# Optimization experiments

Hardware: AMD Instinct MI355X
Metric: run time of the kernel (lower is better)

The kernel has to match this reference:

```python
import jax, jax.numpy as jnp
import numpy as np

EPS = 1e-5

def _ln(x):
    # non-affine LayerNorm over last dim
    m = jnp.mean(x, axis=-1, keepdims=True)
    v = jnp.var(x, axis=-1, keepdims=True)
    return (x - m) / jnp.sqrt(v + EPS)

def setup_inputs() -> dict:
    key = jax.random.key(0)
    ks = jax.random.split(key, 6)
    B, D_in, H = 16384, 512, 512
    bound_i = 1.0 / np.sqrt(D_in)
    bound_h = 1.0 / np.sqrt(H)
    x = jax.random.normal(ks[0], (B, D_in), dtype=jnp.float32)
    hx = jax.random.normal(ks[1], (B, H), dtype=jnp.float32)
    W_i2h = jax.random.uniform(ks[2], (3 * H, D_in), minval=-bound_i, maxval=bound_i, dtype=jnp.float32)
    b_i2h = jax.random.uniform(ks[3], (3 * H,), minval=-bound_i, maxval=bound_i, dtype=jnp.float32)
    W_h2h = jax.random.uniform(ks[4], (3 * H, H), minval=-bound_h, maxval=bound_h, dtype=jnp.float32)
    b_h2h = jax.random.uniform(ks[5], (3 * H,), minval=-bound_h, maxval=bound_h, dtype=jnp.float32)
    return {"x": x, "hx": hx, "W_i2h": W_i2h, "b_i2h": b_i2h, "W_h2h": W_h2h, "b_h2h": b_h2h}

def reference(x, hx, W_i2h, b_i2h, W_h2h, b_h2h):
    H = hx.shape[-1]
    xt = x @ W_i2h.T + b_i2h        # [B, 3H]
    ht = hx @ W_h2h.T + b_h2h       # [B, 3H]
    x_new = xt[:, 2 * H:]
    h_new = ht[:, 2 * H:]
    gates = jax.nn.sigmoid(_ln(xt[:, : 2 * H]) + _ln(ht[:, : 2 * H]))
    r_t = gates[:, :H]
    z_t = gates[:, H:]
    n_t = jnp.tanh(_ln(x_new) + r_t * _ln(h_new))
    h_t = z_t * hx + (1.0 - z_t) * n_t
    return h_t
```

## Files before the change

### kernel.cpp

```cpp
#include <hip/hip_runtime.h>

#define M_ROWS 16384
#define N_COLS 1536
#define K_DIM  512
#define H_DIM  512

typedef __attribute__((ext_vector_type(8))) short short8;
typedef __attribute__((ext_vector_type(16))) float f32x16;

__device__ __forceinline__ unsigned short f2bf(float f) {
  unsigned u = __float_as_uint(f);
  u += 0x7fffu + ((u >> 16) & 1u);
  return (unsigned short)(u >> 16);
}
__device__ __forceinline__ float bf2f(unsigned short h) {
  return __uint_as_float(((unsigned)h) << 16);
}
__device__ __forceinline__ unsigned cvt_pk_bf16(float lo, float hi) {
  unsigned r;
  asm("v_cvt_pk_bf16_f32 %0, %1, %2" : "=v"(r) : "v"(lo), "v"(hi));
  return r;
}

__device__ __forceinline__ void gload_lds16(const void* g, void* l) {
  __builtin_amdgcn_global_load_lds((const __attribute__((address_space(1))) void*)g,
                                   (__attribute__((address_space(3))) void*)l,
                                   16, 0, 0);
}

__global__ __launch_bounds__(256) void cvt_w(
    const float* __restrict__ Wi, const float* __restrict__ Wh,
    unsigned short* __restrict__ Wib, unsigned short* __restrict__ Whb) {
  int i = blockIdx.x * blockDim.x + threadIdx.x;
  const float* s; unsigned short* d; int off;
  if (i < 196608) { s = Wi; d = Wib; off = i; }
  else            { s = Wh; d = Whb; off = i - 196608; }
  float4 f = ((const float4*)s)[off];
  ushort4 u;
  u.x = f2bf(f.x); u.y = f2bf(f.y); u.z = f2bf(f.z); u.w = f2bf(f.w);
  ((ushort4*)d)[off] = u;
}

__global__ __launch_bounds__(512, 1) void fused(
    const float* __restrict__ x, const float* __restrict__ hx,
    const unsigned short* __restrict__ Wib, const unsigned short* __restrict__ Whb,
    const float* __restrict__ b_i2h, const float* __restrict__ b_h2h,
    unsigned short* __restrict__ xt, unsigned short* __restrict__ ht,
    float* __restrict__ out) {
  const int m0 = blockIdx.x * 64;

  __shared__ short ldsA[8][64][64];
  __shared__ short ldsB[512 * 64];

  const int t = threadIdx.x;
  const int w = t >> 6, lane = t & 63;
  const int l31 = lane & 31, h = lane >> 5;
  const int srow = lane >> 3;
  const int scol = ((lane & 7) ^ srow) * 8;

  for (int mat = 0; mat < 2; ++mat) {
    const float* A32         = mat ? hx : x;
    const unsigned short* Bw = mat ? Whb : Wib;
    const float* bias        = mat ? b_h2h : b_i2h;
    unsigned short* outp     = mat ? ht : xt;

    __syncthreads();
    {
      const int arow = t >> 3, ac = t & 7;
      const int pc = (ac ^ (arow & 7)) * 8;
#pragma unroll
      for (int kt = 0; kt < 8; ++kt) {
        const float* src = A32 + (size_t)(m0 + arow) * K_DIM + kt * 64 + ac * 8;
        float4 f0 = *(const float4*)src;
        float4 f1 = *(const float4*)(src + 4);
        uint4 u;
        u.x = cvt_pk_bf16(f0.x, f0.y);
        u.y = cvt_pk_bf16(f0.z, f0.w);
        u.z = cvt_pk_bf16(f1.x, f1.y);
        u.w = cvt_pk_bf16(f1.z, f1.w);
        *(uint4*)&ldsA[kt][arow][pc] = u;
      }
    }

    for (int p = 0; p < 3; ++p) {
      const int n0 = p * 512;
      f32x16 acc[2][2];
#pragma unroll
      for (int i = 0; i < 2; ++i)
#pragma unroll
        for (int j = 0; j < 2; ++j)
#pragma unroll
          for (int r = 0; r < 16; ++r) acc[i][j][r] = 0.f;

      for (int kt = 0; kt < 8; ++kt) {
        __syncthreads();
#pragma unroll
        for (int q = 0; q < 8; ++q) {
          const int br = w * 64 + q * 8;
          gload_lds16(Bw + (size_t)(n0 + br + srow) * K_DIM + kt * 64 + scol,
                      &ldsB[br * 64]);
        }
        __syncthreads();
#pragma unroll
        for (int kk = 0; kk < 4; ++kk) {
          const int chunk = ((kk * 2 + h) ^ (l31 & 7)) * 8;
          short8 af[2], bfr[2];
#pragma unroll
          for (int i = 0; i < 2; ++i)
            af[i] = *(const short8*)&ldsA[kt][i * 32 + l31][chunk];
#pragma unroll
          for (int j = 0; j < 2; ++j)
            bfr[j] = *(const short8*)&ldsB[(w * 64 + j * 32 + l31) * 64 + chunk];
#pragma unroll
          for (int i = 0; i < 2; ++i)
#pragma unroll
            for (int j = 0; j < 2; ++j)
              acc[i][j] = __builtin_amdgcn_mfma_f32_32x32x16_bf16(af[i], bfr[j], acc[i][j], 0, 0, 0);
        }
      }

      const float biasj0 = bias[n0 + w * 64 + l31];
      const float biasj1 = bias[n0 + w * 64 + 32 + l31];
#pragma unroll
      for (int i = 0; i < 2; ++i) {
#pragma unroll
        for (int g = 0; g < 4; ++g) {
#pragma unroll
          for (int d = 0; d < 4; ++d) {
            const int reg = g * 4 + d;
            const int row = d + 8 * g + 4 * h;
            ushort2 pk;
            pk.x = f2bf(acc[i][0][reg] + biasj0);
            pk.y = f2bf(acc[i][1][reg] + biasj1);
            *(ushort2*)(outp + (size_t)(m0 + i * 32 + row) * N_COLS +
                        n0 + w * 64 + 2 * l31) = pk;
          }
        }
      }
      __syncthreads();
    }
  }

  __threadfence_block();
  __syncthreads();

  const int base4 = 64 * (lane >> 3) + 4 * (lane & 7);
#pragma unroll 1
  for (int rr = 0; rr < 8; ++rr) {
    const int b = m0 + w * 8 + rr;
    const size_t rb = (size_t)b * N_COLS;

    const short8 sxr = *(const short8*)&xt[rb + 8 * lane];
    const short8 sxz = *(const short8*)&xt[rb + 512 + 8 * lane];
    const short8 sxn = *(const short8*)&xt[rb + 1024 + 8 * lane];
    const short8 shr = *(const short8*)&ht[rb + 8 * lane];
    const short8 shz = *(const short8*)&ht[rb + 512 + 8 * lane];
    const short8 shn = *(const short8*)&ht[rb + 1024 + 8 * lane];
    const float* hxrow = hx + (size_t)b * H_DIM;
    const float4 hx0 = *(const float4*)&hxrow[base4];
    const float4 hx1 = *(const float4*)&hxrow[base4 + 32];

    float pr[8] = {0.f, 0.f, 0.f, 0.f, 0.f, 0.f, 0.f, 0.f};
#pragma unroll
    for (int k = 0; k < 8; ++k) {
      const float xr = bf2f((unsigned short)sxr[k]);
      const float xz = bf2f((unsigned short)sxz[k]);
      const float xn = bf2f((unsigned short)sxn[k]);
      const float hr = bf2f((unsigned short)shr[k]);
      const float hz = bf2f((unsigned short)shz[k]);
      const float hn = bf2f((unsigned short)shn[k]);
      pr[0] += xr + xz;
      pr[1] += xr * xr + xz * xz;
      pr[2] += xn;
      pr[3] += xn * xn;
      pr[4] += hr + hz;
      pr[5] += hr * hr + hz * hz;
      pr[6] += hn;
      pr[7] += hn * hn;
    }
#pragma unroll
    for (int msk = 1; msk < 64; msk <<= 1)
#pragma unroll
      for (int k = 0; k < 8; ++k) pr[k] += __shfl_xor(pr[k], msk);

    const float inv2H = 1.f / 1024.f, invH = 1.f / 512.f;
    const float mx0 = pr[0] * inv2H;
    const float ix0 = rsqrtf(pr[1] * inv2H - mx0 * mx0 + 1e-5f);
    const float mx1 = pr[2] * invH;
    const float ix1 = rsqrtf(pr[3] * invH - mx1 * mx1 + 1e-5f);
    const float mh0 = pr[4] * inv2H;
    const float ih0 = rsqrtf(pr[5] * inv2H - mh0 * mh0 + 1e-5f);
    const float mh1 = pr[6] * invH;
    const float ih1 = rsqrtf(pr[7] * invH - mh1 * mh1 + 1e-5f);

    auto calc = [&](float xrv, float xzv, float xnv, float hrv, float hzv,
                    float hnv, float hxs) -> float {
      float ar = (xrv - mx0) * ix0 + (hrv - mh0) * ih0;
      float az = (xzv - mx0) * ix0 + (hzv - mh0) * ih0;
      float r = 1.f / (1.f + __expf(-ar));
      float z = 1.f / (1.f + __expf(-az));
      float arg = (xnv - mx1) * ix1 + r * ((hnv - mh1) * ih1);
      float e2 = __expf(2.f * arg);
      float nn = (e2 - 1.f) / (e2 + 1.f);
      return z * hxs + (1.f - z) * nn;
    };

    float* orow = out + (size_t)b * H_DIM;
    float4 r0, r1;
    float* r0p = (float*)&r0;
    float* r1p = (float*)&r1;
    const float* h0p = (const float*)&hx0;
    const float* h1p = (const float*)&hx1;
#pragma unroll
    for (int k = 0; k < 4; ++k) {
      r0p[k] = calc(bf2f((unsigned short)sxr[2 * k]), bf2f((unsigned short)sxz[2 * k]),
                    bf2f((unsigned short)sxn[2 * k]), bf2f((unsigned short)shr[2 * k]),
                    bf2f((unsigned short)shz[2 * k]), bf2f((unsigned short)shn[2 * k]),
                    h0p[k]);
      r1p[k] = calc(bf2f((unsigned short)sxr[2 * k + 1]), bf2f((unsigned short)sxz[2 * k + 1]),
                    bf2f((unsigned short)sxn[2 * k + 1]), bf2f((unsigned short)shr[2 * k + 1]),
                    bf2f((unsigned short)shz[2 * k + 1]), bf2f((unsigned short)shn[2 * k + 1]),
                    h1p[k]);
    }
    *(float4*)&orow[base4] = r0;
    *(float4*)&orow[base4 + 32] = r1;
  }
}

extern "C" void kernel_launch(void* const* d_in, const int* in_sizes, int n_in,
                              void* d_out, int out_size, void* d_ws, size_t ws_size,
                              hipStream_t stream) {
  const float* x  = (const float*)d_in[0];
  const float* hx = (const float*)d_in[1];
  const float* Wi = (const float*)d_in[2];
  const float* bi = (const float*)d_in[3];
  const float* Wh = (const float*)d_in[4];
  const float* bh = (const float*)d_in[5];
  float* out = (float*)d_out;

  char* ws = (char*)d_ws;
  unsigned short* Wib = (unsigned short*)(ws);
  unsigned short* Whb = (unsigned short*)(ws + 1572864);
  unsigned short* xt  = (unsigned short*)(ws + 3145728);
  unsigned short* ht  = (unsigned short*)(ws + 53477376);

  cvt_w<<<1536, 256, 0, stream>>>(Wi, Wh, Wib, Whb);

  fused<<<256, 512, 0, stream>>>(x, hx, Wib, Whb, bi, bh, xt, ht, out);
}
```

Measured before the change: 219.5 us.

## Halve row tile to 32, run two blocks per CU, reuse hx from LDS

The fused GEMM+GRU kernel now processes 32 rows per 256-thread block over six 256-column passes, instead of 64 rows per 512-thread block. The launch bound allows two blocks per CU so one block's MFMA work can overlap another's loads and barriers. The per-k-tile barrier now sits after the compute, which removes one sync per tile. The epilogue reads hx from the bf16 copy already staged in LDS instead of reloading fp32 hx from global memory. In exchange, each block reloads the weights for half as many rows, so weight traffic doubles, and the final blend uses a bf16-rounded hx.

```diff
diff --git a/kernel.cpp b/kernel.cpp
--- a/kernel.cpp
+++ b/kernel.cpp
@@ -41,16 +41,16 @@
   ((ushort4*)d)[off] = u;
 }
 
-__global__ __launch_bounds__(512, 1) void fused(
+__global__ __launch_bounds__(256, 2) void fused(
     const float* __restrict__ x, const float* __restrict__ hx,
     const unsigned short* __restrict__ Wib, const unsigned short* __restrict__ Whb,
     const float* __restrict__ b_i2h, const float* __restrict__ b_h2h,
     unsigned short* __restrict__ xt, unsigned short* __restrict__ ht,
     float* __restrict__ out) {
-  const int m0 = blockIdx.x * 64;
-
-  __shared__ short ldsA[8][64][64];
-  __shared__ short ldsB[512 * 64];
+  const int m0 = blockIdx.x * 32;
+
+  __shared__ short ldsA[8][32][64];
+  __shared__ short ldsB[256 * 64];
 
   const int t = threadIdx.x;
   const int w = t >> 6, lane = t & 63;
@@ -81,19 +81,17 @@
         *(uint4*)&ldsA[kt][arow][pc] = u;
       }
     }
-
-    for (int p = 0; p < 3; ++p) {
-      const int n0 = p * 512;
-      f32x16 acc[2][2];
-#pragma unroll
-      for (int i = 0; i < 2; ++i)
-#pragma unroll
-        for (int j = 0; j < 2; ++j)
-#pragma unroll
-          for (int r = 0; r < 16; ++r) acc[i][j][r] = 0.f;
+    __syncthreads();
+
+    for (int nc = 0; nc < 6; ++nc) {
+      const int n0 = nc * 256;
+      f32x16 acc[2];
+#pragma unroll
+      for (int j = 0; j < 2; ++j)
+#pragma unroll
+        for (int r = 0; r < 16; ++r) acc[j][r] = 0.f;
 
       for (int kt = 0; kt < 8; ++kt) {
-        __syncthreads();
 #pragma unroll
         for (int q = 0; q < 8; ++q) {
           const int br = w * 64 + q * 8;
@@ -104,40 +102,33 @@
 #pragma unroll
         for (int kk = 0; kk < 4; ++kk) {
           const int chunk = ((kk * 2 + h) ^ (l31 & 7)) * 8;
-          short8 af[2], bfr[2];
-#pragma unroll
-          for (int i = 0; i < 2; ++i)
-            af[i] = *(const short8*)&ldsA[kt][i * 32 + l31][chunk];
+          const short8 af = *(const short8*)&ldsA[kt][l31][chunk];
+          short8 bfr[2];
 #pragma unroll
           for (int j = 0; j < 2; ++j)
             bfr[j] = *(const short8*)&ldsB[(w * 64 + j * 32 + l31) * 64 + chunk];
 #pragma unroll
-          for (int i = 0; i < 2; ++i)
-#pragma unroll
-            for (int j = 0; j < 2; ++j)
-              acc[i][j] = __builtin_amdgcn_mfma_f32_32x32x16_bf16(af[i], bfr[j], acc[i][j], 0, 0, 0);
+          for (int j = 0; j < 2; ++j)
+            acc[j] = __builtin_amdgcn_mfma_f32_32x32x16_bf16(af, bfr[j], acc[j], 0, 0, 0);
+        }
+        __syncthreads();
+      }
+
+      const int nbase = n0 + w * 64;
+      const float biasj0 = bias[nbase + l31];
+      const float biasj1 = bias[nbase + 32 + l31];
+#pragma unroll
+      for (int g = 0; g < 4; ++g) {
+#pragma unroll
+        for (int d = 0; d < 4; ++d) {
+          const int reg = g * 4 + d;
+          const int row = d + 8 * g + 4 * h;
+          ushort2 pk;
+          pk.x = f2bf(acc[0][reg] + biasj0);
+          pk.y = f2bf(acc[1][reg] + biasj1);
+          *(ushort2*)(outp + (size_t)(m0 + row) * N_COLS + nbase + 2 * l31) = pk;
         }
       }
-
-      const float biasj0 = bias[n0 + w * 64 + l31];
-      const float biasj1 = bias[n0 + w * 64 + 32 + l31];
-#pragma unroll
-      for (int i = 0; i < 2; ++i) {
-#pragma unroll
-        for (int g = 0; g < 4; ++g) {
-#pragma unroll
-          for (int d = 0; d < 4; ++d) {
-            const int reg = g * 4 + d;
-            const int row = d + 8 * g + 4 * h;
-            ushort2 pk;
-            pk.x = f2bf(acc[i][0][reg] + biasj0);
-            pk.y = f2bf(acc[i][1][reg] + biasj1);
-            *(ushort2*)(outp + (size_t)(m0 + i * 32 + row) * N_COLS +
-                        n0 + w * 64 + 2 * l31) = pk;
-          }
-        }
-      }
-      __syncthreads();
     }
   }
 
@@ -145,9 +136,13 @@
   __syncthreads();
 
   const int base4 = 64 * (lane >> 3) + 4 * (lane & 7);
+  const int kti = lane >> 3;
+  const int jj  = (lane & 7) >> 1;
+  const int e0  = (lane & 1) * 4;
 #pragma unroll 1
   for (int rr = 0; rr < 8; ++rr) {
-    const int b = m0 + w * 8 + rr;
+    const int rl = w * 8 + rr;
+    const int b  = m0 + rl;
     const size_t rb = (size_t)b * N_COLS;
 
     const short8 sxr = *(const short8*)&xt[rb + 8 * lane];
@@ -156,9 +151,8 @@
     const short8 shr = *(const short8*)&ht[rb + 8 * lane];
     const short8 shz = *(const short8*)&ht[rb + 512 + 8 * lane];
     const short8 shn = *(const short8*)&ht[rb + 1024 + 8 * lane];
-    const float* hxrow = hx + (size_t)b * H_DIM;
-    const float4 hx0 = *(const float4*)&hxrow[base4];
-    const float4 hx1 = *(const float4*)&hxrow[base4 + 32];
+    const ushort4 hx0u = *(const ushort4*)&ldsA[kti][rl][(jj ^ (rl & 7)) * 8 + e0];
+    const ushort4 hx1u = *(const ushort4*)&ldsA[kti][rl][((jj + 4) ^ (rl & 7)) * 8 + e0];
 
     float pr[8] = {0.f, 0.f, 0.f, 0.f, 0.f, 0.f, 0.f, 0.f};
 #pragma unroll
@@ -209,18 +203,18 @@
     float4 r0, r1;
     float* r0p = (float*)&r0;
     float* r1p = (float*)&r1;
-    const float* h0p = (const float*)&hx0;
-    const float* h1p = (const float*)&hx1;
+    const unsigned short hx0a[4] = {hx0u.x, hx0u.y, hx0u.z, hx0u.w};
+    const unsigned short hx1a[4] = {hx1u.x, hx1u.y, hx1u.z, hx1u.w};
 #pragma unroll
     for (int k = 0; k < 4; ++k) {
       r0p[k] = calc(bf2f((unsigned short)sxr[2 * k]), bf2f((unsigned short)sxz[2 * k]),
                     bf2f((unsigned short)sxn[2 * k]), bf2f((unsigned short)shr[2 * k]),
                     bf2f((unsigned short)shz[2 * k]), bf2f((unsigned short)shn[2 * k]),
-                    h0p[k]);
+                    bf2f(hx0a[k]));
       r1p[k] = calc(bf2f((unsigned short)sxr[2 * k + 1]), bf2f((unsigned short)sxz[2 * k + 1]),
                     bf2f((unsigned short)sxn[2 * k + 1]), bf2f((unsigned short)shr[2 * k + 1]),
                     bf2f((unsigned short)shz[2 * k + 1]), bf2f((unsigned short)shn[2 * k + 1]),
-                    h1p[k]);
+                    bf2f(hx1a[k]));
     }
     *(float4*)&orow[base4] = r0;
     *(float4*)&orow[base4 + 32] = r1;
@@ -246,5 +240,5 @@
 
   cvt_w<<<1536, 256, 0, stream>>>(Wi, Wh, Wib, Whb);
 
-  fused<<<256, 512, 0, stream>>>(x, hx, Wib, Whb, bi, bh, xt, ht, out);
-}
+  fused<<<512, 256, 0, stream>>>(x, hx, Wib, Whb, bi, bh, xt, ht, out);
+}
```

After: 224.2 us. 2.1% more time.
